# Optimization experiments

Measured on AMD Instinct MI355X. Metric: run time of the kernel, lower is better.

The kernel has to match this reference:

```python
import jax, jax.numpy as jnp
import numpy as np

CHANNEL = 256
MEM_SIZE = 684
POS_NUM = 128
NEG_NUM = 512
TEMP = 1.0
CLASS_NUM = 60
BANK_ROWS = MEM_SIZE * CLASS_NUM  # 41040
BATCH = 512


def setup_inputs() -> dict:
    key = jax.random.key(0)
    k1, k2, k3, k4 = jax.random.split(key, 4)
    f = jax.random.normal(k1, (BATCH, CHANNEL), dtype=jnp.float32)
    f_normed = f / jnp.linalg.norm(f, axis=-1, keepdims=True)
    label = jax.random.randint(k2, (BATCH,), 0, CLASS_NUM, dtype=jnp.int32)
    bank = jax.random.normal(k3, (BANK_ROWS, CHANNEL), dtype=jnp.float32)
    bank = bank / jnp.linalg.norm(bank, axis=-1, keepdims=True)
    bank_flag = jnp.ones((BANK_ROWS,), dtype=jnp.float32)  # warmed-up bank
    rand_neg = jax.random.uniform(k4, (BATCH, BANK_ROWS), dtype=jnp.float32)
    # exact torch roundrobin enqueue logic (sequential over the batch)
    rr = np.zeros(CLASS_NUM, dtype=np.int64)
    idxs = []
    for i in np.asarray(label).tolist():
        rr[i] = rr[i] + 1 if rr[i] < CLASS_NUM - 1 else 0
        idxs.append(int(rr[i]) + i * MEM_SIZE)
    enqueue_idx = jnp.asarray(idxs, dtype=jnp.int32)
    return {"f_normed": f_normed, "label": label, "enqueue_idx": enqueue_idx,
            "bank": bank, "bank_flag": bank_flag, "rand_neg": rand_neg}


def reference(f_normed, label, enqueue_idx, bank, bank_flag, rand_neg):
    N = f_normed.shape[0]
    # enqueue (detached write, as in torch: Bank[indies] = f_normed.detach())
    bank = bank.at[enqueue_idx].set(jax.lax.stop_gradient(f_normed))
    flag = bank_flag.at[enqueue_idx].set(1.0)
    # all_pairs: [N, M]
    all_pairs = jnp.einsum('nc,mc->nm', f_normed, bank)
    bank_label = jnp.tile(jnp.arange(CLASS_NUM), MEM_SIZE)  # arange(C).repeat(mem)
    eq = label[:, None] == bank_label[None, :]
    valid = flag > 0
    pos_mask = eq & valid
    neg_mask = (~eq) & valid
    # hard positives: smallest POS_NUM positive similarities per row
    pos_hard = jnp.sort(jnp.where(pos_mask, all_pairs, jnp.inf), axis=-1)[:, :POS_NUM]
    # hard negatives: largest NEG_NUM negative similarities per row
    neg_hard, _ = jax.lax.top_k(jnp.where(neg_mask, all_pairs, -jnp.inf), NEG_NUM)
    # random negatives: uniform sample without replacement via noise argsort
    r = jnp.where(neg_mask, rand_neg, jnp.inf)
    rand_idx = jnp.argsort(r, axis=-1)[:, :NEG_NUM]
    neg_rand = jnp.take_along_axis(all_pairs, rand_idx, axis=-1)
    # combined logits: [N, 2*POS_NUM, 1+NEG_NUM]
    pos = pos_hard[:, :, None]
    h2h = jnp.concatenate([pos, jnp.broadcast_to(neg_hard[:, None, :], (N, POS_NUM, NEG_NUM))], axis=-1)
    h2r = jnp.concatenate([pos, jnp.broadcast_to(neg_rand[:, None, :], (N, POS_NUM, NEG_NUM))], axis=-1)
    combined = jnp.concatenate([h2h, h2r], axis=1).reshape(-1, 1 + NEG_NUM)
    # cross entropy with target class 0 for every row
    loss = -jnp.mean(jax.nn.log_softmax(combined / TEMP, axis=-1)[:, 0])
    return loss
```

## Files before the change

### kernel.cpp

```cpp
#include <hip/hip_runtime.h>

#define CH    256
#define MEM   684
#define POSN  128
#define NEGN  512
#define CLS   60
#define ROWS  41040
#define BATCHN 512

typedef unsigned int u32;
typedef unsigned short u16;
typedef unsigned long long u64;

typedef __attribute__((ext_vector_type(8))) short bf16x8;
typedef __attribute__((ext_vector_type(4))) float f32x4;

__device__ __forceinline__ float b2f(u16 u) { return __uint_as_float(((u32)u) << 16); }
__device__ __forceinline__ u16 f2b(float x) {
  u32 u = __float_as_uint(x);
  u32 r = ((u >> 16) & 1u) + 0x7FFFu;
  return (u16)((u + r) >> 16);
}
__device__ __forceinline__ u32 umin2(u32 a, u32 b) { return a < b ? a : b; }

#if defined(__has_builtin)
#if __has_builtin(__builtin_amdgcn_global_load_lds)
#define HAVE_GLL 1
#endif
#endif

__device__ __forceinline__ void stage16(const u16* g, u16* l) {
#ifdef HAVE_GLL
  __builtin_amdgcn_global_load_lds((const __attribute__((address_space(1))) void*)g,
                                   (__attribute__((address_space(3))) void*)l, 16, 0, 0);
#else
  *(uint4*)l = *(const uint4*)g;
#endif
}

__global__ __launch_bounds__(256) void k_convert(const float* __restrict__ bank,
                                                 u16* __restrict__ bankB) {
  size_t i = (size_t)(blockIdx.x * 256 + threadIdx.x) * 8;
  float4 a = *(const float4*)(bank + i);
  float4 b = *(const float4*)(bank + i + 4);
  uint4 o;
  o.x = (u32)f2b(a.x) | ((u32)f2b(a.y) << 16);
  o.y = (u32)f2b(a.z) | ((u32)f2b(a.w) << 16);
  o.z = (u32)f2b(b.x) | ((u32)f2b(b.y) << 16);
  o.w = (u32)f2b(b.z) | ((u32)f2b(b.w) << 16);
  *(uint4*)(bankB + i) = o;
}

__global__ __launch_bounds__(256) void k_scatter(const float* __restrict__ f,
                                                 const int* __restrict__ enq,
                                                 u16* __restrict__ fB,
                                                 u16* __restrict__ bankB) {
  int n = blockIdx.x, t = threadIdx.x;
  u16 v = f2b(f[n * CH + t]);
  fB[n * CH + t] = v;
  int row = enq[n];
  bankB[(size_t)row * CH + t] = v;
}

__global__ __launch_bounds__(256) void k_gemm(const u16* __restrict__ fB,
                                              const u16* __restrict__ bankB,
                                              u16* __restrict__ Cb) {
  __shared__ __align__(16) u16 As[128 * 32];
  __shared__ __align__(16) u16 Bs[128 * 32];
  const int tid = threadIdx.x;
  const int wave = tid >> 6, lane = tid & 63;
  const int bm = blockIdx.x * 128;
  const int bn = blockIdx.y * 128;
  const int wm = (wave & 1) * 64, wn = (wave >> 1) * 64;
  const int m_in = lane & 15;
  const int ks = (lane >> 4) * 8;

  f32x4 acc[4][4] = {};

  for (int k0 = 0; k0 < CH; k0 += 32) {
    __syncthreads();
#pragma unroll
    for (int i = 0; i < 2; i++) {
      int u = tid + 256 * i;
      int row = u >> 2;
      int kk = (u & 3) * 8;
      stage16(fB + (size_t)(bm + row) * CH + k0 + kk, As + u * 8);
      int rb = bn + row;
      if (rb >= ROWS) rb = bn;
      stage16(bankB + (size_t)rb * CH + k0 + kk, Bs + u * 8);
    }
    __syncthreads();

    bf16x8 af[4], bf[4];
#pragma unroll
    for (int t4 = 0; t4 < 4; t4++) {
      af[t4] = *(const bf16x8*)(As + (wm + t4 * 16 + m_in) * 32 + ks);
      bf[t4] = *(const bf16x8*)(Bs + (wn + t4 * 16 + m_in) * 32 + ks);
    }
#pragma unroll
    for (int mi = 0; mi < 4; mi++)
#pragma unroll
      for (int ni = 0; ni < 4; ni++)
        acc[mi][ni] = __builtin_amdgcn_mfma_f32_16x16x32_bf16(af[mi], bf[ni], acc[mi][ni], 0, 0, 0);
  }

  const int rr = (lane >> 4) * 4;
  const int cc = lane & 15;
#pragma unroll
  for (int mi = 0; mi < 4; mi++) {
#pragma unroll
    for (int ni = 0; ni < 4; ni++) {
      int ncol = bn + wn + ni * 16 + cc;
      if (ncol < ROWS) {
        size_t base = (size_t)(bm + wm + mi * 16 + rr) * ROWS + ncol;
#pragma unroll
        for (int q = 0; q < 4; q++) Cb[base + (size_t)q * ROWS] = f2b(acc[mi][ni][q]);
      }
    }
  }
}

__device__ __forceinline__ u32 scanN(u32 v, u32* tmp, int tid) {
  tmp[tid] = v;
  __syncthreads();
  for (int off = 1; off < 1024; off <<= 1) {
    u32 t = (tid >= off) ? tmp[tid - off] : 0u;
    __syncthreads();
    tmp[tid] += t;
    __syncthreads();
  }
  return tmp[tid];
}

__device__ __forceinline__ float redsum1024(float v, float* tmp, int tid) {
  tmp[tid] = v;
  __syncthreads();
  for (int off = 512; off > 0; off >>= 1) {
    if (tid < off) tmp[tid] += tmp[tid + off];
    __syncthreads();
  }
  float r = tmp[0];
  __syncthreads();
  return r;
}

__device__ __forceinline__ int binof(float v, float lo, float scale) {
  int b = (int)((v - lo) * scale);
  return b < 0 ? 0 : (b > 2047 ? 2047 : b);
}

__device__ __forceinline__ u32 wave_append(u32* cnt, bool pred) {
  u64 mask = __ballot(pred);
  u32 ret = 0xFFFFFFFFu;
  if (pred) {
    int lane = (int)(threadIdx.x & 63);
    int leader = __ffsll((u64)mask) - 1;
    u32 base = 0;
    if (lane == leader) base = atomicAdd(cnt, (u32)__popcll(mask));
    base = __shfl(base, leader, 64);
    ret = base + (u32)__popcll(mask & ((1ull << lane) - 1ull));
  }
  return ret;
}

#define VITER 5
#define VTAIL 80
#define VTAILBASE 40960
#define CAPC 3072
#define CAPR 1536

__global__ __launch_bounds__(1024) void k_select(const u16* __restrict__ Cb,
                                                 const float* __restrict__ rnd,
                                                 const int* __restrict__ label,
                                                 float* __restrict__ partial) {
  const int n = blockIdx.x;
  const int tid = threadIdx.x;
  const u16* crow = Cb + (size_t)n * ROWS;
  const float* rrow = rnd + (size_t)n * ROWS;
  const int lab = label[n];

  __shared__ __align__(16) char smem[56448];
  u32* histc = (u32*)(smem);
  u32* histr = (u32*)(smem + 8192);
  float* clist = (float*)(smem + 16384);
  float* rl_rv = (float*)(smem + 28672);
  float* rl_cv = (float*)(smem + 34816);
  u32* rl_mi = (u32*)(smem + 40960);
  u32* stmp = (u32*)(smem + 47104);
  float* fred = (float*)(smem + 47104);
  float* cb_c = (float*)(smem + 51200);
  float* rb_r = (float*)(smem + 53248);
  float* rb_c = (float*)(smem + 54272);
  u32* rb_m = (u32*)(smem + 55296);
  u32* ctl = (u32*)(smem + 56320);
  float* bc_f = (float*)(ctl + 8);
  float* posv = clist;

  const int rv0 = (tid * 8) % 60;

  float T1 = 0.09375f;
  float T0 = 0.03125f;
  u32 F = 0, G = 0;
  float sc_c, sc_r;

  for (int attempt = 0;; attempt++) {
    for (int i = tid; i < 2048; i += 1024) { histc[i] = 0; histr[i] = 0; }
    if (tid == 0) { ctl[0] = 0; ctl[1] = 0; }
    __syncthreads();
    sc_c = 2048.0f / (1.0625f - T1);
    sc_r = 2048.0f / T0;
    int rb = rv0;
    for (int it = 0; it < VITER; it++) {
      int m8 = (it * 1024 + tid) * 8;
      uint4 cr = *(const uint4*)(crow + m8);
      float4 ra = *(const float4*)(rrow + m8);
      float4 rb4 = *(const float4*)(rrow + m8 + 4);
      u32 cw[4] = {cr.x, cr.y, cr.z, cr.w};
      float rs[8] = {ra.x, ra.y, ra.z, ra.w, rb4.x, rb4.y, rb4.z, rb4.w};
      int r = rb;
#pragma unroll
      for (int j = 0; j < 8; j++) {
        bool isneg = (r != lab);
        float c = b2f((u16)(cw[j >> 1] >> ((j & 1) * 16)));
        bool pc = isneg && (c > T1);
        u32 p1 = wave_append(&ctl[0], pc);
        if (pc) {
          if (p1 < CAPC) clist[p1] = c;
          atomicAdd(&histc[binof(c, T1, sc_c)], 1u);
        }
        float rv = rs[j];
        bool pr = isneg && (rv < T0);
        u32 p2 = wave_append(&ctl[1], pr);
        if (pr) {
          if (p2 < CAPR) { rl_rv[p2] = rv; rl_cv[p2] = c; rl_mi[p2] = (u32)(m8 + j); }
          atomicAdd(&histr[binof(rv, 0.0f, sc_r)], 1u);
        }
        r++;
        if (r == 60) r = 0;
      }
      rb += 32;
      if (rb >= 60) rb -= 60;
    }
    if (tid < VTAIL) {
      int m = VTAILBASE + tid;
      int r = 40 + tid;
      if (r >= 60) r -= 60;
      bool isneg = (r != lab);
      float c = b2f(crow[m]);
      bool pc = isneg && (c > T1);
      u32 p1 = wave_append(&ctl[0], pc);
      if (pc) {
        if (p1 < CAPC) clist[p1] = c;
        atomicAdd(&histc[binof(c, T1, sc_c)], 1u);
      }
      float rv = rrow[m];
      bool pr = isneg && (rv < T0);
      u32 p2 = wave_append(&ctl[1], pr);
      if (pr) {
        if (p2 < CAPR) { rl_rv[p2] = rv; rl_cv[p2] = c; rl_mi[p2] = (u32)m; }
        atomicAdd(&histr[binof(rv, 0.0f, sc_r)], 1u);
      }
    }
    __syncthreads();
    F = ctl[0];
    G = ctl[1];
    __syncthreads();
    if (F >= NEGN && G >= NEGN) break;
    if (F < NEGN) T1 = -1.1f;
    if (G < NEGN) T0 = 1.1f;
  }
  const bool listc_ok = (F <= CAPC);
  const bool listr_ok = (G <= CAPR);

  if (tid == 0) { ctl[2] = 0; ctl[3] = 0; ctl[4] = 0; ctl[5] = 0; ctl[6] = 0; ctl[7] = 0; }
  u32 fsum = histc[tid * 2] + histc[tid * 2 + 1];
  u32 finc = scanN(fsum, stmp, tid);
  u32 fexc = finc - fsum;
  u32 tcpos = F - NEGN + 1;
  if (fexc < tcpos && tcpos <= finc) {
    u32 run = fexc;
#pragma unroll
    for (int i = 0; i < 2; i++) {
      u32 h = histc[tid * 2 + i];
      if (run + h >= tcpos) { ctl[4] = (u32)(tid * 2 + i); ctl[5] = F - (run + h); break; }
      run += h;
    }
  }
  __syncthreads();
  const u32 b_c = ctl[4], cnt_gt = ctl[5];

  u32 gsum = histr[tid * 2] + histr[tid * 2 + 1];
  u32 ginc = scanN(gsum, stmp, tid);
  u32 gexc = ginc - gsum;
  if (gexc < NEGN && NEGN <= ginc) {
    u32 run = gexc;
#pragma unroll
    for (int i = 0; i < 2; i++) {
      u32 h = histr[tid * 2 + i];
      if (run + h >= NEGN) { ctl[6] = (u32)(tid * 2 + i); ctl[7] = run; break; }
      run += h;
    }
  }
  __syncthreads();
  const u32 b_r = ctl[6], cnt_lt = ctl[7];
  const u32 need_c = NEGN - cnt_gt;
  const u32 need_r = NEGN - cnt_lt;

  float sH = 0.f, sR = 0.f;
  if (listc_ok) {
    for (u32 i = tid; i < F; i += 1024) {
      float c = clist[i];
      u32 b = (u32)binof(c, T1, sc_c);
      if (b > b_c) sH += expf(c);
      else if (b == b_c) {
        u32 id = atomicAdd(&ctl[2], 1u);
        if (id < 512) cb_c[id] = c;
      }
    }
  }
  if (listr_ok) {
    for (u32 i = tid; i < G; i += 1024) {
      float rv = rl_rv[i];
      u32 b = (u32)binof(rv, 0.0f, sc_r);
      if (b < b_r) sR += expf(rl_cv[i]);
      else if (b == b_r) {
        u32 id = atomicAdd(&ctl[3], 1u);
        if (id < 256) { rb_r[id] = rv; rb_c[id] = rl_cv[i]; rb_m[id] = rl_mi[i]; }
      }
    }
  }
  if (!listc_ok || !listr_ok) {
    for (int m = tid; m < ROWS; m += 1024) {
      int r = m % 60;
      if (r == lab) continue;
      float c = b2f(crow[m]);
      if (!listc_ok && c > T1) {
        u32 b = (u32)binof(c, T1, sc_c);
        if (b > b_c) sH += expf(c);
        else if (b == b_c) {
          u32 id = atomicAdd(&ctl[2], 1u);
          if (id < 512) cb_c[id] = c;
        }
      }
      if (!listr_ok) {
        float rv = rrow[m];
        if (rv < T0) {
          u32 b = (u32)binof(rv, 0.0f, sc_r);
          if (b < b_r) sR += expf(c);
          else if (b == b_r) {
            u32 id = atomicAdd(&ctl[3], 1u);
            if (id < 256) { rb_r[id] = rv; rb_c[id] = c; rb_m[id] = (u32)m; }
          }
        }
      }
    }
  }
  __syncthreads();
  float SHsum = redsum1024(sH, fred, tid);
  float SRsum = redsum1024(sR, fred, tid);

  if (tid == 0) {
    float addH = 0.f;
    u32 Lc = umin2(ctl[2], 512u);
    u32 kc = umin2(need_c, Lc);
    for (u32 k = 0; k < kc; k++) {
      int best = 0;
      float bv = -3.0e38f;
      for (u32 i = 0; i < Lc; i++)
        if (cb_c[i] > bv) { bv = cb_c[i]; best = (int)i; }
      cb_c[best] = -3.0e38f;
      addH += expf(bv);
    }
    u32 Lr = umin2(ctl[3], 256u);
    for (u32 i = 1; i < Lr; i++) {
      float rv = rb_r[i]; u32 mm = rb_m[i]; float cv = rb_c[i];
      int j = (int)i - 1;
      while (j >= 0 && (rb_r[j] > rv || (rb_r[j] == rv && rb_m[j] > mm))) {
        rb_r[j + 1] = rb_r[j]; rb_m[j + 1] = rb_m[j]; rb_c[j + 1] = rb_c[j];
        j--;
      }
      rb_r[j + 1] = rv; rb_m[j + 1] = mm; rb_c[j + 1] = cv;
    }
    float addR = 0.f;
    u32 kr = umin2(need_r, Lr);
    for (u32 i = 0; i < kr; i++) addR += expf(rb_c[i]);
    bc_f[0] = addH;
    bc_f[1] = addR;
  }
  __syncthreads();
  const float S_H = SHsum + bc_f[0];
  const float S_R = SRsum + bc_f[1];
  __syncthreads();

  posv[tid] = (tid < MEM) ? b2f(crow[lab + CLS * tid]) : INFINITY;
  __syncthreads();
  for (u32 k = 2; k <= 1024; k <<= 1) {
    for (u32 j = k >> 1; j > 0; j >>= 1) {
      u32 i = (u32)tid;
      u32 ix = i ^ j;
      if (ix > i) {
        float a = posv[i], b = posv[ix];
        bool up = ((i & k) == 0);
        if ((a > b) == up) { posv[i] = b; posv[ix] = a; }
      }
      __syncthreads();
    }
  }

  float term = 0.f;
  if (tid < POSN) {
    float p = posv[tid];
    float e = expf(p);
    term = (p - logf(e + S_H)) + (p - logf(e + S_R));
  }
  float tot = redsum1024(term, fred, tid);
  if (tid == 0) partial[n] = tot;
}

__global__ __launch_bounds__(256) void k_final(const float* __restrict__ partial,
                                               float* __restrict__ out) {
  __shared__ float fred[256];
  int tid = threadIdx.x;
  float v = partial[tid] + partial[tid + 256];
  fred[tid] = v;
  __syncthreads();
  for (int off = 128; off > 0; off >>= 1) {
    if (tid < off) fred[tid] += fred[tid + off];
    __syncthreads();
  }
  if (tid == 0) out[0] = -fred[0] / (float)(BATCHN * 2 * POSN);
}

extern "C" void kernel_launch(void* const* d_in, const int* in_sizes, int n_in,
                              void* d_out, int out_size, void* d_ws, size_t ws_size,
                              hipStream_t stream) {
  const float* f = (const float*)d_in[0];
  const int* label = (const int*)d_in[1];
  const int* enq = (const int*)d_in[2];
  const float* bank = (const float*)d_in[3];
  const float* rnd = (const float*)d_in[5];
  float* out = (float*)d_out;

  char* ws = (char*)d_ws;
  u16* bankB = (u16*)ws;
  u16* fB = (u16*)(ws + 21012480);
  u16* Cb = (u16*)(ws + 21012480 + 262144);
  float* partial = (float*)(ws + 21012480 + 262144 + 42024960);

  k_convert<<<dim3(5130), dim3(256), 0, stream>>>(bank, bankB);
  k_scatter<<<dim3(BATCHN), dim3(256), 0, stream>>>(f, enq, fB, bankB);
  k_gemm<<<dim3(4, 321), dim3(256), 0, stream>>>(fB, bankB, Cb);
  k_select<<<dim3(BATCHN), dim3(1024), 0, stream>>>(Cb, rnd, label, partial);
  k_final<<<dim3(1), dim3(256), 0, stream>>>(partial, out);
}
```

Baseline: 244.6 us.

## Move candidate filtering into GEMM epilogue and separate random-noise prefilter kernel

The GEMM epilogue now collects hard-negative candidates above the threshold into per-row global lists, staging them in shared memory first. A new kernel prefilters the random-noise row into compact (value, index) lists. The select kernel then builds its histograms from these small lists instead of rescanning the full similarity and noise rows, and it falls back to a full scan only when a list is too short or overflows. It also replaces the shared-memory scans, reductions and the bitonic sort with wave shuffles and folds the final reduction into an atomicAdd, which makes the summation order nondeterministic and adds epilogue atomics to the GEMM.

Result: slower. 275.4 us (+12.6%).

```diff
diff --git a/kernel.cpp b/kernel.cpp
--- a/kernel.cpp
+++ b/kernel.cpp
@@ -7,6 +7,12 @@
 #define CLS   60
 #define ROWS  41040
 #define BATCHN 512
+
+#define T1F 0.09375f
+#define T0F 0.03125f
+#define CAPCL 4096
+#define CAPRL 2048
+#define CSTG  48
 
 typedef unsigned int u32;
 typedef unsigned short u16;
@@ -54,99 +60,15 @@
 __global__ __launch_bounds__(256) void k_scatter(const float* __restrict__ f,
                                                  const int* __restrict__ enq,
                                                  u16* __restrict__ fB,
-                                                 u16* __restrict__ bankB) {
+                                                 u16* __restrict__ bankB,
+                                                 u32* __restrict__ gccnt,
+                                                 u32* __restrict__ grcnt) {
   int n = blockIdx.x, t = threadIdx.x;
   u16 v = f2b(f[n * CH + t]);
   fB[n * CH + t] = v;
   int row = enq[n];
   bankB[(size_t)row * CH + t] = v;
-}
-
-__global__ __launch_bounds__(256) void k_gemm(const u16* __restrict__ fB,
-                                              const u16* __restrict__ bankB,
-                                              u16* __restrict__ Cb) {
-  __shared__ __align__(16) u16 As[128 * 32];
-  __shared__ __align__(16) u16 Bs[128 * 32];
-  const int tid = threadIdx.x;
-  const int wave = tid >> 6, lane = tid & 63;
-  const int bm = blockIdx.x * 128;
-  const int bn = blockIdx.y * 128;
-  const int wm = (wave & 1) * 64, wn = (wave >> 1) * 64;
-  const int m_in = lane & 15;
-  const int ks = (lane >> 4) * 8;
-
-  f32x4 acc[4][4] = {};
-
-  for (int k0 = 0; k0 < CH; k0 += 32) {
-    __syncthreads();
-#pragma unroll
-    for (int i = 0; i < 2; i++) {
-      int u = tid + 256 * i;
-      int row = u >> 2;
-      int kk = (u & 3) * 8;
-      stage16(fB + (size_t)(bm + row) * CH + k0 + kk, As + u * 8);
-      int rb = bn + row;
-      if (rb >= ROWS) rb = bn;
-      stage16(bankB + (size_t)rb * CH + k0 + kk, Bs + u * 8);
-    }
-    __syncthreads();
-
-    bf16x8 af[4], bf[4];
-#pragma unroll
-    for (int t4 = 0; t4 < 4; t4++) {
-      af[t4] = *(const bf16x8*)(As + (wm + t4 * 16 + m_in) * 32 + ks);
-      bf[t4] = *(const bf16x8*)(Bs + (wn + t4 * 16 + m_in) * 32 + ks);
-    }
-#pragma unroll
-    for (int mi = 0; mi < 4; mi++)
-#pragma unroll
-      for (int ni = 0; ni < 4; ni++)
-        acc[mi][ni] = __builtin_amdgcn_mfma_f32_16x16x32_bf16(af[mi], bf[ni], acc[mi][ni], 0, 0, 0);
-  }
-
-  const int rr = (lane >> 4) * 4;
-  const int cc = lane & 15;
-#pragma unroll
-  for (int mi = 0; mi < 4; mi++) {
-#pragma unroll
-    for (int ni = 0; ni < 4; ni++) {
-      int ncol = bn + wn + ni * 16 + cc;
-      if (ncol < ROWS) {
-        size_t base = (size_t)(bm + wm + mi * 16 + rr) * ROWS + ncol;
-#pragma unroll
-        for (int q = 0; q < 4; q++) Cb[base + (size_t)q * ROWS] = f2b(acc[mi][ni][q]);
-      }
-    }
-  }
-}
-
-__device__ __forceinline__ u32 scanN(u32 v, u32* tmp, int tid) {
-  tmp[tid] = v;
-  __syncthreads();
-  for (int off = 1; off < 1024; off <<= 1) {
-    u32 t = (tid >= off) ? tmp[tid - off] : 0u;
-    __syncthreads();
-    tmp[tid] += t;
-    __syncthreads();
-  }
-  return tmp[tid];
-}
-
-__device__ __forceinline__ float redsum1024(float v, float* tmp, int tid) {
-  tmp[tid] = v;
-  __syncthreads();
-  for (int off = 512; off > 0; off >>= 1) {
-    if (tid < off) tmp[tid] += tmp[tid + off];
-    __syncthreads();
-  }
-  float r = tmp[0];
-  __syncthreads();
-  return r;
-}
-
-__device__ __forceinline__ int binof(float v, float lo, float scale) {
-  int b = (int)((v - lo) * scale);
-  return b < 0 ? 0 : (b > 2047 ? 2047 : b);
+  if (t == 0) { gccnt[n] = 0; grcnt[n] = 0; }
 }
 
 __device__ __forceinline__ u32 wave_append(u32* cnt, bool pred) {
@@ -166,115 +88,274 @@
 #define VITER 5
 #define VTAIL 80
 #define VTAILBASE 40960
-#define CAPC 3072
-#define CAPR 1536
+
+__global__ __launch_bounds__(1024) void k_rfilter(const float* __restrict__ rnd,
+                                                  const int* __restrict__ label,
+                                                  float* __restrict__ grl,
+                                                  u32* __restrict__ grcnt) {
+  const int n = blockIdx.x;
+  const int tid = threadIdx.x;
+  const float* rrow = rnd + (size_t)n * ROWS;
+  const int lab = label[n];
+  __shared__ u32 cnt;
+  if (tid == 0) cnt = 0;
+  __syncthreads();
+  float* outbase = grl + (size_t)n * CAPRL * 2;
+  int rb = (tid * 8) % 60;
+  for (int it = 0; it < VITER; it++) {
+    int m8 = (it * 1024 + tid) * 8;
+    float4 a = *(const float4*)(rrow + m8);
+    float4 b = *(const float4*)(rrow + m8 + 4);
+    float rs[8] = {a.x, a.y, a.z, a.w, b.x, b.y, b.z, b.w};
+    int r = rb;
+#pragma unroll
+    for (int j = 0; j < 8; j++) {
+      bool pred = (r != lab) && (rs[j] < T0F);
+      u32 slot = wave_append(&cnt, pred);
+      if (pred && slot < CAPRL) {
+        float2 p;
+        p.x = rs[j];
+        p.y = __uint_as_float((u32)(m8 + j));
+        *(float2*)(outbase + slot * 2) = p;
+      }
+      r++;
+      if (r == 60) r = 0;
+    }
+    rb += 32;
+    if (rb >= 60) rb -= 60;
+  }
+  if (tid < VTAIL) {
+    int m = VTAILBASE + tid;
+    int r = 40 + tid;
+    if (r >= 60) r -= 60;
+    float rv = rrow[m];
+    bool pred = (r != lab) && (rv < T0F);
+    u32 slot = wave_append(&cnt, pred);
+    if (pred && slot < CAPRL) {
+      float2 p;
+      p.x = rv;
+      p.y = __uint_as_float((u32)m);
+      *(float2*)(outbase + slot * 2) = p;
+    }
+  }
+  __syncthreads();
+  if (tid == 0) grcnt[n] = cnt;
+}
+
+__global__ __launch_bounds__(256) void k_gemm(const u16* __restrict__ fB,
+                                              const u16* __restrict__ bankB,
+                                              const int* __restrict__ label,
+                                              u16* __restrict__ Cb,
+                                              float* __restrict__ gclist,
+                                              u32* __restrict__ gccnt) {
+  __shared__ __align__(16) u16 As[128 * 32];
+  __shared__ __align__(16) u16 Bs[128 * 32];
+  __shared__ float cstage[128 * CSTG];
+  __shared__ u32 ccnt_l[128];
+  __shared__ int lab_l[128];
+  const int tid = threadIdx.x;
+  const int wave = tid >> 6, lane = tid & 63;
+  const int bm = blockIdx.x * 128;
+  const int bn = blockIdx.y * 128;
+  const int wm = (wave & 1) * 64, wn = (wave >> 1) * 64;
+  const int m_in = lane & 15;
+  const int ks = (lane >> 4) * 8;
+
+  if (tid < 128) { ccnt_l[tid] = 0; lab_l[tid] = label[bm + tid]; }
+
+  f32x4 acc[4][4] = {};
+
+  for (int k0 = 0; k0 < CH; k0 += 32) {
+    __syncthreads();
+#pragma unroll
+    for (int i = 0; i < 2; i++) {
+      int u = tid + 256 * i;
+      int row = u >> 2;
+      int kk = (u & 3) * 8;
+      stage16(fB + (size_t)(bm + row) * CH + k0 + kk, As + u * 8);
+      int rb = bn + row;
+      if (rb >= ROWS) rb = bn;
+      stage16(bankB + (size_t)rb * CH + k0 + kk, Bs + u * 8);
+    }
+    __syncthreads();
+
+    bf16x8 af[4], bf[4];
+#pragma unroll
+    for (int t4 = 0; t4 < 4; t4++) {
+      af[t4] = *(const bf16x8*)(As + (wm + t4 * 16 + m_in) * 32 + ks);
+      bf[t4] = *(const bf16x8*)(Bs + (wn + t4 * 16 + m_in) * 32 + ks);
+    }
+#pragma unroll
+    for (int mi = 0; mi < 4; mi++)
+#pragma unroll
+      for (int ni = 0; ni < 4; ni++)
+        acc[mi][ni] = __builtin_amdgcn_mfma_f32_16x16x32_bf16(af[mi], bf[ni], acc[mi][ni], 0, 0, 0);
+  }
+
+  const int rr = (lane >> 4) * 4;
+  const int cc = lane & 15;
+#pragma unroll
+  for (int ni = 0; ni < 4; ni++) {
+    int ncol = bn + wn + ni * 16 + cc;
+    if (ncol >= ROWS) continue;
+    int ncolmod = ncol % 60;
+#pragma unroll
+    for (int mi = 0; mi < 4; mi++) {
+      int rloc = wm + mi * 16 + rr;
+      size_t base = (size_t)(bm + rloc) * ROWS + ncol;
+#pragma unroll
+      for (int q = 0; q < 4; q++) {
+        u16 cw = f2b(acc[mi][ni][q]);
+        Cb[base + (size_t)q * ROWS] = cw;
+        float c = b2f(cw);
+        int rq = rloc + q;
+        if (c > T1F && ncolmod != lab_l[rq]) {
+          u32 slot = atomicAdd(&ccnt_l[rq], 1u);
+          if (slot < CSTG) {
+            cstage[rq * CSTG + slot] = c;
+          } else {
+            int grow = bm + rq;
+            u32 s2 = atomicAdd(&gccnt[grow], 1u);
+            if (s2 < CAPCL) gclist[(size_t)grow * CAPCL + s2] = c;
+          }
+        }
+      }
+    }
+  }
+  __syncthreads();
+  if (tid < 128) {
+    u32 k = umin2(ccnt_l[tid], CSTG);
+    if (k) {
+      int grow = bm + tid;
+      u32 base = atomicAdd(&gccnt[grow], k);
+      for (u32 i = 0; i < k; i++) {
+        u32 s = base + i;
+        if (s < CAPCL) gclist[(size_t)grow * CAPCL + s] = cstage[tid * CSTG + i];
+      }
+    }
+  }
+}
+
+__device__ __forceinline__ u32 scanN(u32 v, u32* tmp, int tid) {
+  u32 x = v;
+#pragma unroll
+  for (int off = 1; off < 64; off <<= 1) {
+    u32 y = (u32)__shfl_up((int)x, off, 64);
+    if ((tid & 63) >= off) x += y;
+  }
+  if ((tid & 63) == 63) tmp[tid >> 6] = x;
+  __syncthreads();
+  if (tid < 64) {
+    u32 t = (tid < 16) ? tmp[tid] : 0u;
+#pragma unroll
+    for (int off = 1; off < 16; off <<= 1) {
+      u32 y = (u32)__shfl_up((int)t, off, 64);
+      if (tid >= off) t += y;
+    }
+    if (tid < 16) tmp[tid + 16] = t;
+  }
+  __syncthreads();
+  u32 base = (tid >= 64) ? tmp[16 + (tid >> 6) - 1] : 0u;
+  return base + x;
+}
+
+__device__ __forceinline__ float redsum1024(float v, float* tmp, int tid) {
+#pragma unroll
+  for (int off = 32; off > 0; off >>= 1) v += __shfl_xor(v, off, 64);
+  if ((tid & 63) == 0) tmp[tid >> 6] = v;
+  __syncthreads();
+  if (tid < 64) {
+    float t = (tid < 16) ? tmp[tid] : 0.f;
+#pragma unroll
+    for (int off = 8; off > 0; off >>= 1) t += __shfl_xor(t, off, 64);
+    if (tid == 0) tmp[0] = t;
+  }
+  __syncthreads();
+  float r = tmp[0];
+  __syncthreads();
+  return r;
+}
+
+__device__ __forceinline__ int binof(float v, float lo, float scale) {
+  int b = (int)((v - lo) * scale);
+  return b < 0 ? 0 : (b > 2047 ? 2047 : b);
+}
 
 __global__ __launch_bounds__(1024) void k_select(const u16* __restrict__ Cb,
                                                  const float* __restrict__ rnd,
                                                  const int* __restrict__ label,
-                                                 float* __restrict__ partial) {
+                                                 const float* __restrict__ gclist,
+                                                 const float* __restrict__ grl,
+                                                 const u32* __restrict__ gccnt,
+                                                 const u32* __restrict__ grcnt,
+                                                 float* __restrict__ out) {
   const int n = blockIdx.x;
   const int tid = threadIdx.x;
   const u16* crow = Cb + (size_t)n * ROWS;
   const float* rrow = rnd + (size_t)n * ROWS;
   const int lab = label[n];
 
-  __shared__ __align__(16) char smem[56448];
+  __shared__ __align__(16) char smem[62784];
   u32* histc = (u32*)(smem);
   u32* histr = (u32*)(smem + 8192);
-  float* clist = (float*)(smem + 16384);
-  float* rl_rv = (float*)(smem + 28672);
-  float* rl_cv = (float*)(smem + 34816);
-  u32* rl_mi = (u32*)(smem + 40960);
-  u32* stmp = (u32*)(smem + 47104);
-  float* fred = (float*)(smem + 47104);
-  float* cb_c = (float*)(smem + 51200);
-  float* rb_r = (float*)(smem + 53248);
-  float* rb_c = (float*)(smem + 54272);
-  u32* rb_m = (u32*)(smem + 55296);
-  u32* ctl = (u32*)(smem + 56320);
-  float* bc_f = (float*)(ctl + 8);
-  float* posv = clist;
-
-  const int rv0 = (tid * 8) % 60;
-
-  float T1 = 0.09375f;
-  float T0 = 0.03125f;
-  u32 F = 0, G = 0;
-  float sc_c, sc_r;
-
-  for (int attempt = 0;; attempt++) {
-    for (int i = tid; i < 2048; i += 1024) { histc[i] = 0; histr[i] = 0; }
-    if (tid == 0) { ctl[0] = 0; ctl[1] = 0; }
-    __syncthreads();
-    sc_c = 2048.0f / (1.0625f - T1);
-    sc_r = 2048.0f / T0;
-    int rb = rv0;
-    for (int it = 0; it < VITER; it++) {
-      int m8 = (it * 1024 + tid) * 8;
-      uint4 cr = *(const uint4*)(crow + m8);
-      float4 ra = *(const float4*)(rrow + m8);
-      float4 rb4 = *(const float4*)(rrow + m8 + 4);
-      u32 cw[4] = {cr.x, cr.y, cr.z, cr.w};
-      float rs[8] = {ra.x, ra.y, ra.z, ra.w, rb4.x, rb4.y, rb4.z, rb4.w};
-      int r = rb;
-#pragma unroll
-      for (int j = 0; j < 8; j++) {
-        bool isneg = (r != lab);
-        float c = b2f((u16)(cw[j >> 1] >> ((j & 1) * 16)));
-        bool pc = isneg && (c > T1);
-        u32 p1 = wave_append(&ctl[0], pc);
-        if (pc) {
-          if (p1 < CAPC) clist[p1] = c;
-          atomicAdd(&histc[binof(c, T1, sc_c)], 1u);
-        }
-        float rv = rs[j];
-        bool pr = isneg && (rv < T0);
-        u32 p2 = wave_append(&ctl[1], pr);
-        if (pr) {
-          if (p2 < CAPR) { rl_rv[p2] = rv; rl_cv[p2] = c; rl_mi[p2] = (u32)(m8 + j); }
-          atomicAdd(&histr[binof(rv, 0.0f, sc_r)], 1u);
-        }
-        r++;
-        if (r == 60) r = 0;
-      }
-      rb += 32;
-      if (rb >= 60) rb -= 60;
-    }
-    if (tid < VTAIL) {
-      int m = VTAILBASE + tid;
-      int r = 40 + tid;
-      if (r >= 60) r -= 60;
-      bool isneg = (r != lab);
+  float* cl = (float*)(smem + 16384);
+  float* rl_rv = (float*)(smem + 32768);
+  float* rl_cv = (float*)(smem + 40960);
+  u32* rl_mi = (u32*)(smem + 49152);
+  float* cb_c = (float*)(smem + 57344);
+  float* rb_r = (float*)(smem + 59392);
+  float* rb_c = (float*)(smem + 60416);
+  u32* rb_m = (u32*)(smem + 61440);
+  u32* stmp = (u32*)(smem + 62464);
+  float* fred = (float*)(smem + 62592);
+  u32* ctl = (u32*)(smem + 62656);
+  float* bcf = (float*)(ctl + 8);
+  float* posv = cl;
+
+  const u32 Fg = gccnt[n];
+  const u32 Gg = grcnt[n];
+  const bool cok = (Fg >= NEGN && Fg <= CAPCL);
+  const bool rok = (Gg >= NEGN && Gg <= CAPRL);
+  const float T1e = cok ? T1F : -1.1f;
+  const float sc_c = 2048.0f / (cok ? (1.0625f - T1F) : 2.2f);
+  const float sc_r = 2048.0f / (rok ? T0F : 1.1f);
+
+  for (int i = tid; i < 2048; i += 1024) { histc[i] = 0; histr[i] = 0; }
+  if (tid < 16) ctl[tid] = 0;
+  __syncthreads();
+
+  if (cok) {
+    for (u32 i = tid; i < Fg; i += 1024) {
+      float c = gclist[(size_t)n * CAPCL + i];
+      cl[i] = c;
+      atomicAdd(&histc[binof(c, T1e, sc_c)], 1u);
+    }
+  }
+  if (rok) {
+    const float* rbase = grl + (size_t)n * CAPRL * 2;
+    for (u32 i = tid; i < Gg; i += 1024) {
+      float2 p = *(const float2*)(rbase + i * 2);
+      u32 m = __float_as_uint(p.y);
       float c = b2f(crow[m]);
-      bool pc = isneg && (c > T1);
-      u32 p1 = wave_append(&ctl[0], pc);
-      if (pc) {
-        if (p1 < CAPC) clist[p1] = c;
-        atomicAdd(&histc[binof(c, T1, sc_c)], 1u);
-      }
-      float rv = rrow[m];
-      bool pr = isneg && (rv < T0);
-      u32 p2 = wave_append(&ctl[1], pr);
-      if (pr) {
-        if (p2 < CAPR) { rl_rv[p2] = rv; rl_cv[p2] = c; rl_mi[p2] = (u32)m; }
-        atomicAdd(&histr[binof(rv, 0.0f, sc_r)], 1u);
-      }
-    }
-    __syncthreads();
-    F = ctl[0];
-    G = ctl[1];
-    __syncthreads();
-    if (F >= NEGN && G >= NEGN) break;
-    if (F < NEGN) T1 = -1.1f;
-    if (G < NEGN) T0 = 1.1f;
-  }
-  const bool listc_ok = (F <= CAPC);
-  const bool listr_ok = (G <= CAPR);
-
-  if (tid == 0) { ctl[2] = 0; ctl[3] = 0; ctl[4] = 0; ctl[5] = 0; ctl[6] = 0; ctl[7] = 0; }
+      rl_rv[i] = p.x;
+      rl_cv[i] = c;
+      rl_mi[i] = m;
+      atomicAdd(&histr[binof(p.x, 0.0f, sc_r)], 1u);
+    }
+  }
+  if (!cok || !rok) {
+    for (int m = tid; m < ROWS; m += 1024) {
+      int rm = m % 60;
+      if (rm == lab) continue;
+      if (!cok) atomicAdd(&histc[binof(b2f(crow[m]), T1e, sc_c)], 1u);
+      if (!rok) atomicAdd(&histr[binof(rrow[m], 0.0f, sc_r)], 1u);
+    }
+  }
+  __syncthreads();
+
   u32 fsum = histc[tid * 2] + histc[tid * 2 + 1];
   u32 finc = scanN(fsum, stmp, tid);
+  u32 F = stmp[31];
   u32 fexc = finc - fsum;
   u32 tcpos = F - NEGN + 1;
   if (fexc < tcpos && tcpos <= finc) {
@@ -282,13 +363,10 @@
 #pragma unroll
     for (int i = 0; i < 2; i++) {
       u32 h = histc[tid * 2 + i];
-      if (run + h >= tcpos) { ctl[4] = (u32)(tid * 2 + i); ctl[5] = F - (run + h); break; }
+      if (run + h >= tcpos) { ctl[2] = (u32)(tid * 2 + i); ctl[3] = F - (run + h); break; }
       run += h;
     }
   }
-  __syncthreads();
-  const u32 b_c = ctl[4], cnt_gt = ctl[5];
-
   u32 gsum = histr[tid * 2] + histr[tid * 2 + 1];
   u32 ginc = scanN(gsum, stmp, tid);
   u32 gexc = ginc - gsum;
@@ -297,60 +375,59 @@
 #pragma unroll
     for (int i = 0; i < 2; i++) {
       u32 h = histr[tid * 2 + i];
-      if (run + h >= NEGN) { ctl[6] = (u32)(tid * 2 + i); ctl[7] = run; break; }
+      if (run + h >= NEGN) { ctl[4] = (u32)(tid * 2 + i); ctl[5] = run; break; }
       run += h;
     }
   }
   __syncthreads();
-  const u32 b_r = ctl[6], cnt_lt = ctl[7];
+  const u32 b_c = ctl[2], cnt_gt = ctl[3];
+  const u32 b_r = ctl[4], cnt_lt = ctl[5];
   const u32 need_c = NEGN - cnt_gt;
   const u32 need_r = NEGN - cnt_lt;
 
   float sH = 0.f, sR = 0.f;
-  if (listc_ok) {
-    for (u32 i = tid; i < F; i += 1024) {
-      float c = clist[i];
-      u32 b = (u32)binof(c, T1, sc_c);
+  if (cok) {
+    for (u32 i = tid; i < Fg; i += 1024) {
+      float c = cl[i];
+      u32 b = (u32)binof(c, T1e, sc_c);
       if (b > b_c) sH += expf(c);
       else if (b == b_c) {
-        u32 id = atomicAdd(&ctl[2], 1u);
+        u32 id = atomicAdd(&ctl[0], 1u);
         if (id < 512) cb_c[id] = c;
       }
     }
   }
-  if (listr_ok) {
-    for (u32 i = tid; i < G; i += 1024) {
+  if (rok) {
+    for (u32 i = tid; i < Gg; i += 1024) {
       float rv = rl_rv[i];
       u32 b = (u32)binof(rv, 0.0f, sc_r);
       if (b < b_r) sR += expf(rl_cv[i]);
       else if (b == b_r) {
-        u32 id = atomicAdd(&ctl[3], 1u);
+        u32 id = atomicAdd(&ctl[1], 1u);
         if (id < 256) { rb_r[id] = rv; rb_c[id] = rl_cv[i]; rb_m[id] = rl_mi[i]; }
       }
     }
   }
-  if (!listc_ok || !listr_ok) {
+  if (!cok || !rok) {
     for (int m = tid; m < ROWS; m += 1024) {
-      int r = m % 60;
-      if (r == lab) continue;
+      int rm = m % 60;
+      if (rm == lab) continue;
       float c = b2f(crow[m]);
-      if (!listc_ok && c > T1) {
-        u32 b = (u32)binof(c, T1, sc_c);
+      if (!cok) {
+        u32 b = (u32)binof(c, T1e, sc_c);
         if (b > b_c) sH += expf(c);
         else if (b == b_c) {
-          u32 id = atomicAdd(&ctl[2], 1u);
+          u32 id = atomicAdd(&ctl[0], 1u);
           if (id < 512) cb_c[id] = c;
         }
       }
-      if (!listr_ok) {
+      if (!rok) {
         float rv = rrow[m];
-        if (rv < T0) {
-          u32 b = (u32)binof(rv, 0.0f, sc_r);
-          if (b < b_r) sR += expf(c);
-          else if (b == b_r) {
-            u32 id = atomicAdd(&ctl[3], 1u);
-            if (id < 256) { rb_r[id] = rv; rb_c[id] = c; rb_m[id] = (u32)m; }
-          }
+        u32 b = (u32)binof(rv, 0.0f, sc_r);
+        if (b < b_r) sR += expf(c);
+        else if (b == b_r) {
+          u32 id = atomicAdd(&ctl[1], 1u);
+          if (id < 256) { rb_r[id] = rv; rb_c[id] = c; rb_m[id] = (u32)m; }
         }
       }
     }
@@ -361,7 +438,7 @@
 
   if (tid == 0) {
     float addH = 0.f;
-    u32 Lc = umin2(ctl[2], 512u);
+    u32 Lc = umin2(ctl[0], 512u);
     u32 kc = umin2(need_c, Lc);
     for (u32 k = 0; k < kc; k++) {
       int best = 0;
@@ -371,7 +448,7 @@
       cb_c[best] = -3.0e38f;
       addH += expf(bv);
     }
-    u32 Lr = umin2(ctl[3], 256u);
+    u32 Lr = umin2(ctl[1], 256u);
     for (u32 i = 1; i < Lr; i++) {
       float rv = rb_r[i]; u32 mm = rb_m[i]; float cv = rb_c[i];
       int j = (int)i - 1;
@@ -384,51 +461,41 @@
     float addR = 0.f;
     u32 kr = umin2(need_r, Lr);
     for (u32 i = 0; i < kr; i++) addR += expf(rb_c[i]);
-    bc_f[0] = addH;
-    bc_f[1] = addR;
-  }
-  __syncthreads();
-  const float S_H = SHsum + bc_f[0];
-  const float S_R = SRsum + bc_f[1];
-  __syncthreads();
-
-  posv[tid] = (tid < MEM) ? b2f(crow[lab + CLS * tid]) : INFINITY;
-  __syncthreads();
+    bcf[0] = addH;
+    bcf[1] = addR;
+  }
+  __syncthreads();
+  const float S_H = SHsum + bcf[0];
+  const float S_R = SRsum + bcf[1];
+  __syncthreads();
+
+  float v = (tid < MEM) ? b2f(crow[lab + CLS * tid]) : INFINITY;
   for (u32 k = 2; k <= 1024; k <<= 1) {
     for (u32 j = k >> 1; j > 0; j >>= 1) {
-      u32 i = (u32)tid;
-      u32 ix = i ^ j;
-      if (ix > i) {
-        float a = posv[i], b = posv[ix];
-        bool up = ((i & k) == 0);
-        if ((a > b) == up) { posv[i] = b; posv[ix] = a; }
-      }
-      __syncthreads();
+      bool up = ((tid & k) == 0);
+      float pv;
+      if (j >= 64) {
+        posv[tid] = v;
+        __syncthreads();
+        pv = posv[tid ^ j];
+        __syncthreads();
+      } else {
+        pv = __shfl_xor(v, (int)j, 64);
+      }
+      bool lower = ((tid & j) == 0);
+      float mn = fminf(v, pv), mx = fmaxf(v, pv);
+      v = (lower == up) ? mn : mx;
     }
   }
 
   float term = 0.f;
   if (tid < POSN) {
-    float p = posv[tid];
+    float p = v;
     float e = expf(p);
     term = (p - logf(e + S_H)) + (p - logf(e + S_R));
   }
   float tot = redsum1024(term, fred, tid);
-  if (tid == 0) partial[n] = tot;
-}
-
-__global__ __launch_bounds__(256) void k_final(const float* __restrict__ partial,
-                                               float* __restrict__ out) {
-  __shared__ float fred[256];
-  int tid = threadIdx.x;
-  float v = partial[tid] + partial[tid + 256];
-  fred[tid] = v;
-  __syncthreads();
-  for (int off = 128; off > 0; off >>= 1) {
-    if (tid < off) fred[tid] += fred[tid + off];
-    __syncthreads();
-  }
-  if (tid == 0) out[0] = -fred[0] / (float)(BATCHN * 2 * POSN);
+  if (tid == 0) atomicAdd(out, -tot / (float)(BATCHN * 2 * POSN));
 }
 
 extern "C" void kernel_launch(void* const* d_in, const int* in_sizes, int n_in,
@@ -444,12 +511,16 @@
   char* ws = (char*)d_ws;
   u16* bankB = (u16*)ws;
   u16* fB = (u16*)(ws + 21012480);
-  u16* Cb = (u16*)(ws + 21012480 + 262144);
-  float* partial = (float*)(ws + 21012480 + 262144 + 42024960);
-
+  u16* Cb = (u16*)(ws + 21274624);
+  float* gclist = (float*)(ws + 63299584);
+  float* grl = (float*)(ws + 71688192);
+  u32* gccnt = (u32*)(ws + 80076800);
+  u32* grcnt = (u32*)(ws + 80078848);
+
+  hipMemsetAsync(d_out, 0, sizeof(float), stream);
   k_convert<<<dim3(5130), dim3(256), 0, stream>>>(bank, bankB);
-  k_scatter<<<dim3(BATCHN), dim3(256), 0, stream>>>(f, enq, fB, bankB);
-  k_gemm<<<dim3(4, 321), dim3(256), 0, stream>>>(fB, bankB, Cb);
-  k_select<<<dim3(BATCHN), dim3(1024), 0, stream>>>(Cb, rnd, label, partial);
-  k_final<<<dim3(1), dim3(256), 0, stream>>>(partial, out);
-}
+  k_scatter<<<dim3(BATCHN), dim3(256), 0, stream>>>(f, enq, fB, bankB, gccnt, grcnt);
+  k_rfilter<<<dim3(BATCHN), dim3(1024), 0, stream>>>(rnd, label, grl, grcnt);
+  k_gemm<<<dim3(4, 321), dim3(256), 0, stream>>>(fB, bankB, label, Cb, gclist, gccnt);
+  k_select<<<dim3(BATCHN), dim3(1024), 0, stream>>>(Cb, rnd, label, gclist, grl, gccnt, grcnt, out);
+}
```
